# Kernel tuning notes

Measured on AMD Instinct MI355X. Metric: run time of the kernel, lower is better.

The kernel has to match this reference:

```python
import jax, jax.numpy as jnp
import numpy as np


def setup_inputs() -> dict:
    key = jax.random.key(0)
    k1, k2 = jax.random.split(key)
    B, S, N_IN, RANK = 4, 1024, 1024, 64
    x = jax.random.normal(k1, (B, S, N_IN), dtype=jnp.float32)
    # nn.init.uniform_(projector, -0.05, 0.05)
    projector = jax.random.uniform(k2, (N_IN, RANK), dtype=jnp.float32,
                                   minval=-0.05, maxval=0.05)
    return {"x": x, "projector": projector}


def reference(x, projector):
    # x: [B, S, n_in], projector: [n_in, rank]
    t = jnp.matmul(x, projector)                      # [B, S, r]
    # pairwise squared distances: sum_r (t[b,i,r] - t[b,j,r])^2
    diffs = t[:, :, None, :] - t[:, None, :, :]       # [B, S, S, r]
    return jnp.sum(diffs * diffs, axis=-1)            # [B, S, S]
```

## Files before the change

kernel.cpp:

```cpp
#include <hip/hip_runtime.h>

typedef __attribute__((ext_vector_type(8))) short bf8_t;
typedef __attribute__((ext_vector_type(4))) float f4_t;

static __device__ __forceinline__ short f2bf(float f) {
    union { float f; unsigned u; } v; v.f = f;
    unsigned r = v.u + 0x7fffu + ((v.u >> 16) & 1u);
    return (short)(r >> 16);
}
static __device__ __forceinline__ float bf2f(short s) {
    union { unsigned u; float f; } v;
    v.u = ((unsigned)(unsigned short)s) << 16;
    return v.f;
}

__global__ void __launch_bounds__(512, 2)
proj_kernel(const float* __restrict__ x, const float* __restrict__ P,
            short* __restrict__ t, float* __restrict__ norms)
{
    const int tid  = threadIdx.x;
    const int w    = tid >> 6;
    const int lane = tid & 63;
    const int nr   = lane & 15;
    const int quad = lane >> 4;
    const int row  = blockIdx.x * 16 + nr;

    __shared__ __align__(16) char smem[131072];

    const float* xr = x + (size_t)row * 1024;
    f4_t xv[4][2];
    #pragma unroll
    for (int kt = 0; kt < 4; kt++) {
        const int kb = w * 128 + kt * 32 + quad * 8;
        xv[kt][0] = *(const f4_t*)(xr + kb);
        xv[kt][1] = *(const f4_t*)(xr + kb + 4);
    }

    #pragma unroll 4
    for (int it = 0; it < 16; ++it) {
        const int e  = it * 512 + tid;
        const int g  = e & 15;
        const int kp = e >> 4;
        const f4_t p0 = *(const f4_t*)(P + (size_t)(kp * 2    ) * 64 + g * 4);
        const f4_t p1 = *(const f4_t*)(P + (size_t)(kp * 2 + 1) * 64 + g * 4);
        #pragma unroll
        for (int c = 0; c < 4; ++c) {
            const int m = g * 4 + c;
            const unsigned v = ((unsigned)(unsigned short)f2bf(p1[c]) << 16)
                             |  (unsigned)(unsigned short)f2bf(p0[c]);
            *(unsigned*)(smem + m * 2048 + ((kp * 4) ^ ((m & 7) << 4))) = v;
        }
    }
    __syncthreads();

    f4_t acc[4];
    #pragma unroll
    for (int mt = 0; mt < 4; mt++) acc[mt] = f4_t{0.f, 0.f, 0.f, 0.f};

    #pragma unroll
    for (int kt = 0; kt < 4; kt++) {
        bf8_t bfr;
        #pragma unroll
        for (int j = 0; j < 4; j++) {
            bfr[j]     = f2bf(xv[kt][0][j]);
            bfr[4 + j] = f2bf(xv[kt][1][j]);
        }
        const int colb = w * 256 + kt * 64 + quad * 16;
        #pragma unroll
        for (int mt = 0; mt < 4; mt++) {
            const int m = mt * 16 + nr;
            bf8_t afr = *(const bf8_t*)(smem + m * 2048 + (colb ^ ((nr & 7) << 4)));
            acc[mt] = __builtin_amdgcn_mfma_f32_16x16x32_bf16(afr, bfr, acc[mt], 0, 0, 0);
        }
    }
    __syncthreads();

    float* red = (float*)smem;
    if (w > 0) {
        #pragma unroll
        for (int mt = 0; mt < 4; mt++)
            #pragma unroll
            for (int r = 0; r < 4; r++)
                red[((w - 1) * 16 + mt * 4 + r) * 64 + lane] = acc[mt][r];
    }
    __syncthreads();

    if (w == 0) {
        float nrm = 0.f;
        #pragma unroll
        for (int mt = 0; mt < 4; mt++) {
            float v0 = acc[mt][0], v1 = acc[mt][1], v2 = acc[mt][2], v3 = acc[mt][3];
            #pragma unroll
            for (int wi = 0; wi < 7; wi++) {
                v0 += red[(wi * 16 + mt * 4 + 0) * 64 + lane];
                v1 += red[(wi * 16 + mt * 4 + 1) * 64 + lane];
                v2 += red[(wi * 16 + mt * 4 + 2) * 64 + lane];
                v3 += red[(wi * 16 + mt * 4 + 3) * 64 + lane];
            }
            short s0 = f2bf(v0), s1 = f2bf(v1), s2 = f2bf(v2), s3 = f2bf(v3);
            float b0 = bf2f(s0), b1 = bf2f(s1), b2 = bf2f(s2), b3 = bf2f(s3);
            nrm += b0*b0 + b1*b1 + b2*b2 + b3*b3;
            short4 sv; sv.x = s0; sv.y = s1; sv.z = s2; sv.w = s3;
            *(short4*)(t + (size_t)row * 64 + mt * 16 + quad * 4) = sv;
        }
        nrm += __shfl_xor(nrm, 16);
        nrm += __shfl_xor(nrm, 32);
        if (quad == 0) norms[row] = nrm;
    }
}

__global__ void __launch_bounds__(256, 2)
pairwise_kernel(const short* __restrict__ t, const float* __restrict__ norms,
                float* __restrict__ out)
{
    const int b    = blockIdx.y;
    const int ti   = blockIdx.x >> 4;
    const int tj   = blockIdx.x & 15;
    const int tid  = threadIdx.x;
    const int w    = tid >> 6;
    const int lane = tid & 63;
    const int wy   = w >> 1, wx = w & 1;
    const int i0   = ti * 128 + wy * 64;
    const int j0   = tj * 64  + wx * 32;
    const int nr   = lane & 15, quad = lane >> 4;

    __shared__ float ni[128], nj[64];
    if (tid < 128)      ni[tid]       = norms[b * 1024 + ti * 128 + tid];
    else if (tid < 192) nj[tid - 128] = norms[b * 1024 + tj * 64 + (tid - 128)];
    __syncthreads();

    const short* tb = t + (size_t)b * 1024 * 64;

    f4_t acc[4][2];
    #pragma unroll
    for (int ia = 0; ia < 4; ia++)
        #pragma unroll
        for (int jb = 0; jb < 2; jb++) acc[ia][jb] = f4_t{0.f, 0.f, 0.f, 0.f};

    #pragma unroll
    for (int kt = 0; kt < 2; kt++) {
        const int kb = kt * 32 + quad * 8;
        bf8_t A[2], B[4];
        #pragma unroll
        for (int jb = 0; jb < 2; jb++)
            A[jb] = *(const bf8_t*)(tb + (size_t)(j0 + jb * 16 + nr) * 64 + kb);
        #pragma unroll
        for (int ia = 0; ia < 4; ia++)
            B[ia] = *(const bf8_t*)(tb + (size_t)(i0 + ia * 16 + nr) * 64 + kb);
        #pragma unroll
        for (int ia = 0; ia < 4; ia++)
            #pragma unroll
            for (int jb = 0; jb < 2; jb++)
                acc[ia][jb] = __builtin_amdgcn_mfma_f32_16x16x32_bf16(A[jb], B[ia], acc[ia][jb], 0, 0, 0);
    }

    #pragma unroll
    for (int ia = 0; ia < 4; ia++) {
        const int i = i0 + ia * 16 + nr;
        const float niv = ni[wy * 64 + ia * 16 + nr];
        float* orow = out + ((size_t)b * 1024 + i) * 1024 + tj * 64;
        #pragma unroll
        for (int jb = 0; jb < 2; jb++) {
            const int jo = wx * 32 + jb * 16 + quad * 4;
            const float4 nv = *(const float4*)&nj[jo];
            f4_t a = acc[ia][jb];
            float4 v;
            v.x = niv + nv.x - 2.f * a[0];
            v.y = niv + nv.y - 2.f * a[1];
            v.z = niv + nv.z - 2.f * a[2];
            v.w = niv + nv.w - 2.f * a[3];
            *(float4*)(orow + jo) = v;
        }
    }
}

extern "C" void kernel_launch(void* const* d_in, const int* in_sizes, int n_in,
                              void* d_out, int out_size, void* d_ws, size_t ws_size,
                              hipStream_t stream) {
    const float* x = (const float*)d_in[0];
    const float* P = (const float*)d_in[1];
    float* out = (float*)d_out;

    short* t     = (short*)d_ws;
    float* norms = (float*)((char*)d_ws + 512 * 1024);

    proj_kernel<<<256, 512, 0, stream>>>(x, P, t, norms);
    dim3 g2(128, 4);
    pairwise_kernel<<<g2, 256, 0, stream>>>(t, norms, out);
}
```

Baseline: 83.19 us.

## Fuse projection and pairwise distance into one kernel with recomputed row panels

Replaces the two-kernel pipeline with a single kernel. Each block owns a 128x128 output tile, projects its two 128-row panels of x into LDS as bf16 with their norms, then runs the pairwise MFMA and writes the output. This removes the second launch and the workspace round trip for t and norms. In exchange, x is read redundantly: each row panel is re-projected by 8 blocks, so global reads of x grow roughly eightfold (about 128 MB), and the projection work is duplicated. A block-index swizzle is added to improve L2 reuse.

```diff
diff --git a/kernel.cpp b/kernel.cpp
--- a/kernel.cpp
+++ b/kernel.cpp
@@ -2,6 +2,7 @@
 
 typedef __attribute__((ext_vector_type(8))) short bf8_t;
 typedef __attribute__((ext_vector_type(4))) float f4_t;
+typedef __attribute__((ext_vector_type(4))) int   i4_t;
 
 static __device__ __forceinline__ short f2bf(float f) {
     union { float f; unsigned u; } v; v.f = f;
@@ -15,155 +16,147 @@
 }
 
 __global__ void __launch_bounds__(512, 2)
-proj_kernel(const float* __restrict__ x, const float* __restrict__ P,
-            short* __restrict__ t, float* __restrict__ norms)
+fused_kernel(const float* __restrict__ x, const float* __restrict__ P,
+             float* __restrict__ out)
 {
     const int tid  = threadIdx.x;
     const int w    = tid >> 6;
     const int lane = tid & 63;
     const int nr   = lane & 15;
     const int quad = lane >> 4;
-    const int row  = blockIdx.x * 16 + nr;
 
-    __shared__ __align__(16) char smem[131072];
+    const int swz = (blockIdx.x & 7) * 32 + (blockIdx.x >> 3);
+    const int b   = swz >> 6;
+    const int ti  = (swz >> 3) & 7;
+    const int tj  = swz & 7;
 
-    const float* xr = x + (size_t)row * 1024;
-    f4_t xv[4][2];
+    __shared__ __align__(16) char  p_lds[32768];
+    __shared__ __align__(16) short t_lds[2][128][64];
+    __shared__ float nrm_lds[2][128];
+
+    const int pan     = w >> 2;
+    const int wl      = w & 3;
+    const int panbase = (pan ? tj : ti) * 128;
+
+    const float* xr0 = x + (size_t)(b * 1024 + panbase + wl * 32 + nr) * 1024;
+    const float* xr1 = xr0 + (size_t)16 * 1024;
+
+    f4_t acc[2][4];
     #pragma unroll
-    for (int kt = 0; kt < 4; kt++) {
-        const int kb = w * 128 + kt * 32 + quad * 8;
-        xv[kt][0] = *(const f4_t*)(xr + kb);
-        xv[kt][1] = *(const f4_t*)(xr + kb + 4);
+    for (int tt = 0; tt < 2; tt++)
+        #pragma unroll
+        for (int mt = 0; mt < 4; mt++) acc[tt][mt] = f4_t{0.f, 0.f, 0.f, 0.f};
+
+    for (int c = 0; c < 4; ++c) {
+        f4_t xv0[8][2], xv1[8][2];
+        #pragma unroll
+        for (int kt = 0; kt < 8; ++kt) {
+            const int kb = c * 256 + kt * 32 + quad * 8;
+            xv0[kt][0] = *(const f4_t*)(xr0 + kb);
+            xv0[kt][1] = *(const f4_t*)(xr0 + kb + 4);
+            xv1[kt][0] = *(const f4_t*)(xr1 + kb);
+            xv1[kt][1] = *(const f4_t*)(xr1 + kb + 4);
+        }
+        #pragma unroll
+        for (int it = 0; it < 4; ++it) {
+            const int idx = it * 512 + tid;
+            const int m   = idx & 63;
+            const int ks  = idx >> 6;
+            const float* ps = P + (size_t)(c * 256 + ks * 8) * 64 + m;
+            int d0, d1, d2, d3;
+            d0 = ((int)(unsigned short)f2bf(ps[1 * 64]) << 16) | (unsigned short)f2bf(ps[0 * 64]);
+            d1 = ((int)(unsigned short)f2bf(ps[3 * 64]) << 16) | (unsigned short)f2bf(ps[2 * 64]);
+            d2 = ((int)(unsigned short)f2bf(ps[5 * 64]) << 16) | (unsigned short)f2bf(ps[4 * 64]);
+            d3 = ((int)(unsigned short)f2bf(ps[7 * 64]) << 16) | (unsigned short)f2bf(ps[6 * 64]);
+            *(i4_t*)(p_lds + m * 512 + ((ks * 16) ^ ((m & 7) << 4))) = i4_t{d0, d1, d2, d3};
+        }
+        __syncthreads();
+        #pragma unroll
+        for (int kt = 0; kt < 8; ++kt) {
+            const int colb = (kt * 64 + quad * 16) ^ ((nr & 7) << 4);
+            bf8_t afr[4];
+            #pragma unroll
+            for (int mt = 0; mt < 4; ++mt)
+                afr[mt] = *(const bf8_t*)(p_lds + (mt * 16 + nr) * 512 + colb);
+            bf8_t b0, b1;
+            #pragma unroll
+            for (int j = 0; j < 4; ++j) {
+                b0[j] = f2bf(xv0[kt][0][j]); b0[4 + j] = f2bf(xv0[kt][1][j]);
+                b1[j] = f2bf(xv1[kt][0][j]); b1[4 + j] = f2bf(xv1[kt][1][j]);
+            }
+            #pragma unroll
+            for (int mt = 0; mt < 4; ++mt)
+                acc[0][mt] = __builtin_amdgcn_mfma_f32_16x16x32_bf16(afr[mt], b0, acc[0][mt], 0, 0, 0);
+            #pragma unroll
+            for (int mt = 0; mt < 4; ++mt)
+                acc[1][mt] = __builtin_amdgcn_mfma_f32_16x16x32_bf16(afr[mt], b1, acc[1][mt], 0, 0, 0);
+        }
+        __syncthreads();
     }
 
-    #pragma unroll 4
-    for (int it = 0; it < 16; ++it) {
-        const int e  = it * 512 + tid;
-        const int g  = e & 15;
-        const int kp = e >> 4;
-        const f4_t p0 = *(const f4_t*)(P + (size_t)(kp * 2    ) * 64 + g * 4);
-        const f4_t p1 = *(const f4_t*)(P + (size_t)(kp * 2 + 1) * 64 + g * 4);
+    #pragma unroll
+    for (int tt = 0; tt < 2; ++tt) {
+        const int srow = wl * 32 + tt * 16 + nr;
+        char* trow = (char*)t_lds[pan] + srow * 128;
+        float nrm = 0.f;
         #pragma unroll
-        for (int c = 0; c < 4; ++c) {
-            const int m = g * 4 + c;
-            const unsigned v = ((unsigned)(unsigned short)f2bf(p1[c]) << 16)
-                             |  (unsigned)(unsigned short)f2bf(p0[c]);
-            *(unsigned*)(smem + m * 2048 + ((kp * 4) ^ ((m & 7) << 4))) = v;
+        for (int mt = 0; mt < 4; ++mt) {
+            const short s0 = f2bf(acc[tt][mt][0]), s1 = f2bf(acc[tt][mt][1]);
+            const short s2 = f2bf(acc[tt][mt][2]), s3 = f2bf(acc[tt][mt][3]);
+            const float b0 = bf2f(s0), b1 = bf2f(s1), b2 = bf2f(s2), b3 = bf2f(s3);
+            nrm += b0 * b0 + b1 * b1 + b2 * b2 + b3 * b3;
+            uint2 pk;
+            pk.x = ((unsigned)(unsigned short)s1 << 16) | (unsigned short)s0;
+            pk.y = ((unsigned)(unsigned short)s3 << 16) | (unsigned short)s2;
+            *(uint2*)(trow + ((mt * 32 + quad * 8) ^ ((srow & 7) << 4))) = pk;
         }
+        nrm += __shfl_xor(nrm, 16);
+        nrm += __shfl_xor(nrm, 32);
+        if (quad == 0) nrm_lds[pan][srow] = nrm;
     }
     __syncthreads();
 
-    f4_t acc[4];
-    #pragma unroll
-    for (int mt = 0; mt < 4; mt++) acc[mt] = f4_t{0.f, 0.f, 0.f, 0.f};
+    const int wy = w >> 2;
+    const int wx = w & 3;
+    const int i0 = wy * 64, j0 = wx * 32;
 
-    #pragma unroll
-    for (int kt = 0; kt < 4; kt++) {
-        bf8_t bfr;
-        #pragma unroll
-        for (int j = 0; j < 4; j++) {
-            bfr[j]     = f2bf(xv[kt][0][j]);
-            bfr[4 + j] = f2bf(xv[kt][1][j]);
-        }
-        const int colb = w * 256 + kt * 64 + quad * 16;
-        #pragma unroll
-        for (int mt = 0; mt < 4; mt++) {
-            const int m = mt * 16 + nr;
-            bf8_t afr = *(const bf8_t*)(smem + m * 2048 + (colb ^ ((nr & 7) << 4)));
-            acc[mt] = __builtin_amdgcn_mfma_f32_16x16x32_bf16(afr, bfr, acc[mt], 0, 0, 0);
-        }
-    }
-    __syncthreads();
-
-    float* red = (float*)smem;
-    if (w > 0) {
-        #pragma unroll
-        for (int mt = 0; mt < 4; mt++)
-            #pragma unroll
-            for (int r = 0; r < 4; r++)
-                red[((w - 1) * 16 + mt * 4 + r) * 64 + lane] = acc[mt][r];
-    }
-    __syncthreads();
-
-    if (w == 0) {
-        float nrm = 0.f;
-        #pragma unroll
-        for (int mt = 0; mt < 4; mt++) {
-            float v0 = acc[mt][0], v1 = acc[mt][1], v2 = acc[mt][2], v3 = acc[mt][3];
-            #pragma unroll
-            for (int wi = 0; wi < 7; wi++) {
-                v0 += red[(wi * 16 + mt * 4 + 0) * 64 + lane];
-                v1 += red[(wi * 16 + mt * 4 + 1) * 64 + lane];
-                v2 += red[(wi * 16 + mt * 4 + 2) * 64 + lane];
-                v3 += red[(wi * 16 + mt * 4 + 3) * 64 + lane];
-            }
-            short s0 = f2bf(v0), s1 = f2bf(v1), s2 = f2bf(v2), s3 = f2bf(v3);
-            float b0 = bf2f(s0), b1 = bf2f(s1), b2 = bf2f(s2), b3 = bf2f(s3);
-            nrm += b0*b0 + b1*b1 + b2*b2 + b3*b3;
-            short4 sv; sv.x = s0; sv.y = s1; sv.z = s2; sv.w = s3;
-            *(short4*)(t + (size_t)row * 64 + mt * 16 + quad * 4) = sv;
-        }
-        nrm += __shfl_xor(nrm, 16);
-        nrm += __shfl_xor(nrm, 32);
-        if (quad == 0) norms[row] = nrm;
-    }
-}
-
-__global__ void __launch_bounds__(256, 2)
-pairwise_kernel(const short* __restrict__ t, const float* __restrict__ norms,
-                float* __restrict__ out)
-{
-    const int b    = blockIdx.y;
-    const int ti   = blockIdx.x >> 4;
-    const int tj   = blockIdx.x & 15;
-    const int tid  = threadIdx.x;
-    const int w    = tid >> 6;
-    const int lane = tid & 63;
-    const int wy   = w >> 1, wx = w & 1;
-    const int i0   = ti * 128 + wy * 64;
-    const int j0   = tj * 64  + wx * 32;
-    const int nr   = lane & 15, quad = lane >> 4;
-
-    __shared__ float ni[128], nj[64];
-    if (tid < 128)      ni[tid]       = norms[b * 1024 + ti * 128 + tid];
-    else if (tid < 192) nj[tid - 128] = norms[b * 1024 + tj * 64 + (tid - 128)];
-    __syncthreads();
-
-    const short* tb = t + (size_t)b * 1024 * 64;
-
-    f4_t acc[4][2];
+    f4_t pac[4][2];
     #pragma unroll
     for (int ia = 0; ia < 4; ia++)
         #pragma unroll
-        for (int jb = 0; jb < 2; jb++) acc[ia][jb] = f4_t{0.f, 0.f, 0.f, 0.f};
+        for (int jb = 0; jb < 2; jb++) pac[ia][jb] = f4_t{0.f, 0.f, 0.f, 0.f};
 
     #pragma unroll
-    for (int kt = 0; kt < 2; kt++) {
-        const int kb = kt * 32 + quad * 8;
-        bf8_t A[2], B[4];
+    for (int kt = 0; kt < 2; ++kt) {
+        const int colb = kt * 64 + quad * 16;
+        bf8_t A[2], Bv[4];
         #pragma unroll
-        for (int jb = 0; jb < 2; jb++)
-            A[jb] = *(const bf8_t*)(tb + (size_t)(j0 + jb * 16 + nr) * 64 + kb);
+        for (int jb = 0; jb < 2; ++jb) {
+            const int row = j0 + jb * 16 + nr;
+            A[jb] = *(const bf8_t*)((char*)t_lds[1] + row * 128 + (colb ^ ((row & 7) << 4)));
+        }
         #pragma unroll
-        for (int ia = 0; ia < 4; ia++)
-            B[ia] = *(const bf8_t*)(tb + (size_t)(i0 + ia * 16 + nr) * 64 + kb);
+        for (int ia = 0; ia < 4; ++ia) {
+            const int row = i0 + ia * 16 + nr;
+            Bv[ia] = *(const bf8_t*)((char*)t_lds[0] + row * 128 + (colb ^ ((row & 7) << 4)));
+        }
         #pragma unroll
-        for (int ia = 0; ia < 4; ia++)
+        for (int ia = 0; ia < 4; ++ia)
             #pragma unroll
-            for (int jb = 0; jb < 2; jb++)
-                acc[ia][jb] = __builtin_amdgcn_mfma_f32_16x16x32_bf16(A[jb], B[ia], acc[ia][jb], 0, 0, 0);
+            for (int jb = 0; jb < 2; ++jb)
+                pac[ia][jb] = __builtin_amdgcn_mfma_f32_16x16x32_bf16(A[jb], Bv[ia], pac[ia][jb], 0, 0, 0);
     }
 
     #pragma unroll
-    for (int ia = 0; ia < 4; ia++) {
-        const int i = i0 + ia * 16 + nr;
-        const float niv = ni[wy * 64 + ia * 16 + nr];
-        float* orow = out + ((size_t)b * 1024 + i) * 1024 + tj * 64;
+    for (int ia = 0; ia < 4; ++ia) {
+        const int il  = i0 + ia * 16 + nr;
+        const float niv = nrm_lds[0][il];
+        float* orow = out + ((size_t)(b * 1024 + ti * 128 + il)) * 1024 + tj * 128;
         #pragma unroll
-        for (int jb = 0; jb < 2; jb++) {
-            const int jo = wx * 32 + jb * 16 + quad * 4;
-            const float4 nv = *(const float4*)&nj[jo];
-            f4_t a = acc[ia][jb];
+        for (int jb = 0; jb < 2; ++jb) {
+            const int jo = j0 + jb * 16 + quad * 4;
+            const float4 nv = *(const float4*)&nrm_lds[1][jo];
+            f4_t a = pac[ia][jb];
             float4 v;
             v.x = niv + nv.x - 2.f * a[0];
             v.y = niv + nv.y - 2.f * a[1];
@@ -180,11 +173,7 @@
     const float* x = (const float*)d_in[0];
     const float* P = (const float*)d_in[1];
     float* out = (float*)d_out;
+    (void)d_ws; (void)ws_size;
 
-    short* t     = (short*)d_ws;
-    float* norms = (float*)((char*)d_ws + 512 * 1024);
-
-    proj_kernel<<<256, 512, 0, stream>>>(x, P, t, norms);
-    dim3 g2(128, 4);
-    pairwise_kernel<<<g2, 256, 0, stream>>>(t, norms, out);
+    fused_kernel<<<256, 512, 0, stream>>>(x, P, out);
 }
```

Result: slower. 109.6 us (+31.7%).
